# Kernel tuning notes

Measured on AMD Instinct MI355X. Metric: run time of the kernel, lower is better.

The kernel has to match this reference:

```python
import jax, jax.numpy as jnp
import numpy as np
from jax import lax

OUT = 7          # RoIAlign output size (7,7) per module
SR = 2           # sampling ratio (torchvision adaptive -1 made static for jit; see notes)
N_CLASSES = 21
N_ANCHORS = 2


def setup_inputs() -> dict:
    key = jax.random.key(0)
    ks = jax.random.split(key, 20)
    B, C, H, W = 2, 256, 100, 152
    K = 1024
    features = jax.random.normal(ks[0], (B, C, H, W), dtype=jnp.float32)
    # build valid ROIs [batch_idx, x1, y1, x2, y2] in feature-map coords (spatial_scale=1.0)
    bidx = jax.random.randint(ks[1], (K,), 0, B).astype(jnp.float32)
    cx = jax.random.uniform(ks[2], (K,)) * (W - 1)
    cy = jax.random.uniform(ks[3], (K,)) * (H - 1)
    bw = 4.0 + jax.random.uniform(ks[4], (K,)) * 60.0
    bh = 4.0 + jax.random.uniform(ks[5], (K,)) * 60.0
    x1 = jnp.clip(cx - bw / 2, 0.0, W - 1.0)
    x2 = jnp.clip(cx + bw / 2, 0.0, W - 1.0)
    y1 = jnp.clip(cy - bh / 2, 0.0, H - 1.0)
    y2 = jnp.clip(cy + bh / 2, 0.0, H - 1.0)
    rois = jnp.stack([bidx, x1, y1, x2, y2], axis=1)
    s = 0.05
    W1 = jax.random.normal(ks[6], (C, C, 3, 3), dtype=jnp.float32) * s
    b1 = jax.random.normal(ks[7], (C,), dtype=jnp.float32) * s
    W2 = jax.random.normal(ks[8], (C, C, 3, 3), dtype=jnp.float32) * s
    b2 = jax.random.normal(ks[9], (C,), dtype=jnp.float32) * s
    W3 = jax.random.normal(ks[10], (C, C, 3, 3), dtype=jnp.float32) * s
    b3 = jax.random.normal(ks[11], (C,), dtype=jnp.float32) * s
    W4 = jax.random.normal(ks[12], (C, C, 3, 3), dtype=jnp.float32) * s
    b4 = jax.random.normal(ks[13], (C,), dtype=jnp.float32) * s
    W5 = jax.random.normal(ks[14], (N_CLASSES * N_ANCHORS, C, 3, 3), dtype=jnp.float32) * s
    b5 = jax.random.normal(ks[15], (N_CLASSES * N_ANCHORS,), dtype=jnp.float32) * s
    return dict(features=features, rois=rois, W1=W1, b1=b1, W2=W2, b2=b2,
                W3=W3, b3=b3, W4=W4, b4=b4, W5=W5, b5=b5)


def roi_align(feat, rois):
    # feat [B,C,H,W], rois [K,5] -> [K,C,OUT,OUT]; bilinear, aligned=False semantics
    B, C, H, W = feat.shape
    b = rois[:, 0].astype(jnp.int32)                       # [K]
    x1, y1, x2, y2 = rois[:, 1], rois[:, 2], rois[:, 3], rois[:, 4]
    rw = jnp.maximum(x2 - x1, 1.0)
    rh = jnp.maximum(y2 - y1, 1.0)
    # sample point grid: OUT*SR samples per dim, centered in sub-bins
    offs = (jnp.arange(OUT * SR, dtype=feat.dtype) + 0.5) / SR  # in units of bins
    gy = y1[:, None] + offs[None, :] * (rh / OUT)[:, None]      # [K, S]
    gx = x1[:, None] + offs[None, :] * (rw / OUT)[:, None]      # [K, S]
    S = OUT * SR
    yy = jnp.broadcast_to(gy[:, :, None], (gy.shape[0], S, S)).reshape(-1, S * S)  # [K,P]
    xx = jnp.broadcast_to(gx[:, None, :], (gx.shape[0], S, S)).reshape(-1, S * S)
    valid = (yy > -1.0) & (yy < H) & (xx > -1.0) & (xx < W)
    yc = jnp.clip(yy, 0.0, H - 1.0)
    xc = jnp.clip(xx, 0.0, W - 1.0)
    y0 = jnp.clip(jnp.floor(yc), 0.0, H - 2.0)
    x0 = jnp.clip(jnp.floor(xc), 0.0, W - 2.0)
    wy = yc - y0
    wx = xc - x0
    y0i = y0.astype(jnp.int32); y1i = y0i + 1
    x0i = x0.astype(jnp.int32); x1i = x0i + 1
    bb = b[:, None]
    # irregular gathers: [K,P,C] each
    v00 = feat[bb, :, y0i, x0i]
    v01 = feat[bb, :, y0i, x1i]
    v10 = feat[bb, :, y1i, x0i]
    v11 = feat[bb, :, y1i, x1i]
    w00 = ((1 - wy) * (1 - wx))[..., None]
    w01 = ((1 - wy) * wx)[..., None]
    w10 = (wy * (1 - wx))[..., None]
    w11 = (wy * wx)[..., None]
    vals = v00 * w00 + v01 * w01 + v10 * w10 + v11 * w11   # [K,P,C]
    vals = jnp.where(valid[..., None], vals, 0.0)
    K = rois.shape[0]
    vals = vals.reshape(K, OUT, SR, OUT, SR, C).mean(axis=(2, 4))  # [K,OUT,OUT,C]
    return jnp.transpose(vals, (0, 3, 1, 2))               # [K,C,OUT,OUT]


def conv3x3(x, w, bias):
    y = lax.conv_general_dilated(x, w, (1, 1), ((1, 1), (1, 1)),
                                 dimension_numbers=('NCHW', 'OIHW', 'NCHW'))
    return y + bias[None, :, None, None]


def reference(features, rois, W1, b1, W2, b2, W3, b3, W4, b4, W5, b5):
    r = roi_align(features, rois)                # [K,256,7,7]
    h = jax.nn.relu(conv3x3(r, W1, b1))
    h = jax.nn.relu(conv3x3(h, W2, b2))
    h = jax.nn.relu(conv3x3(h, W3, b3))
    h = jax.nn.relu(conv3x3(h, W4, b4))
    out = conv3x3(h, W5, b5)                     # [K, n_classes*2, 7, 7]
    return out
```

## Files before the change

### kernel.cpp

```cpp
#include <hip/hip_runtime.h>
#include <hip/hip_bf16.h>

#define BB   2
#define CC   256
#define HH   100
#define WW   152
#define CO5  42

typedef short short8 __attribute__((ext_vector_type(8)));
typedef float f32x4 __attribute__((ext_vector_type(4)));

typedef unsigned int uint_t;
typedef unsigned short ushort_t;

__device__ __forceinline__ uint_t bf16_rne(float x) {
    uint_t u = __float_as_uint(x);
    return (u + 0x7fffu + ((u >> 16) & 1u)) >> 16;
}
__device__ __forceinline__ void split_bf16(float x, uint_t& h, uint_t& l) {
    h = bf16_rne(x);
    float hf = __uint_as_float(h << 16);
    l = bf16_rne(x - hf);
}

__global__ void ftrans_kernel(const float* __restrict__ f, float* __restrict__ ft) {
    __shared__ float tile[32][33];
    const int x0 = blockIdx.x * 32;
    const int c0 = blockIdx.y * 32;
    const int by = blockIdx.z;
    const int b = by / HH, y = by % HH;
    const int tx = threadIdx.x, ty = threadIdx.y;
    #pragma unroll
    for (int j = 0; j < 4; ++j) {
        int c = c0 + ty + j * 8;
        int x = x0 + tx;
        if (x < WW)
            tile[ty + j * 8][tx] = f[(((size_t)b * CC + c) * HH + y) * WW + x];
    }
    __syncthreads();
    #pragma unroll
    for (int j = 0; j < 4; ++j) {
        int x = x0 + ty + j * 8;
        int c = c0 + tx;
        if (x < WW)
            ft[(((size_t)b * HH + y) * WW + x) * CC + c] = tile[tx][ty + j * 8];
    }
}

__global__ void wprep_kernel(const float* __restrict__ W,
                             ushort_t* __restrict__ wh, ushort_t* __restrict__ wl) {
    int idx = blockIdx.x * 256 + threadIdx.x;
    int tap = idx >> 16;
    int rem = idx & 0xffff;
    int co = rem >> 8, ci = rem & 255;
    float v = W[(size_t)((co << 8) + ci) * 9 + tap];
    uint_t h, l; split_bf16(v, h, l);
    wh[idx] = (ushort_t)h;
    wl[idx] = (ushort_t)l;
}

__global__ void wprep5_kernel(const float* __restrict__ W,
                              ushort_t* __restrict__ wh, ushort_t* __restrict__ wl) {
    int idx = blockIdx.x * 256 + threadIdx.x;
    int tap = idx / 12288;
    int rem = idx % 12288;
    int co = rem >> 8, ci = rem & 255;
    float v = (co < CO5) ? W[(size_t)((co << 8) + ci) * 9 + tap] : 0.0f;
    uint_t h, l; split_bf16(v, h, l);
    wh[idx] = (ushort_t)h;
    wl[idx] = (ushort_t)l;
}

__global__ __launch_bounds__(256) void roialign_kernel(const float* __restrict__ ft,
                                                       const float* __restrict__ rois,
                                                       float* __restrict__ outb) {
    const int roi = blockIdx.x, t = threadIdx.x;
    const float bf = rois[roi * 5 + 0];
    const float x1 = rois[roi * 5 + 1];
    const float y1 = rois[roi * 5 + 2];
    const float x2 = rois[roi * 5 + 3];
    const float y2 = rois[roi * 5 + 4];
    const int b = (int)bf;
    const float rw = fmaxf(x2 - x1, 1.0f);
    const float rh = fmaxf(y2 - y1, 1.0f);
    const float stepy = rh / 7.0f;
    const float stepx = rw / 7.0f;
    const float* base = ft + (size_t)b * HH * WW * CC + t;

    for (int py = 0; py < 7; ++py) {
        for (int px = 0; px < 7; ++px) {
            float s = 0.0f;
            #pragma unroll
            for (int j = 0; j < 4; ++j) {
                const int syi = py * 2 + (j >> 1);
                const int sxi = px * 2 + (j & 1);
                float gy = y1 + ((float)syi + 0.5f) * 0.5f * stepy;
                float gx = x1 + ((float)sxi + 0.5f) * 0.5f * stepx;
                float yc = fminf(fmaxf(gy, 0.0f), (float)(HH - 1));
                float xc = fminf(fmaxf(gx, 0.0f), (float)(WW - 1));
                float y0f = fminf(floorf(yc), (float)(HH - 2));
                float x0f = fminf(floorf(xc), (float)(WW - 2));
                float wy = yc - y0f;
                float wx = xc - x0f;
                int y0 = (int)y0f, x0 = (int)x0f;
                const float* p = base + ((size_t)y0 * WW + x0) * CC;
                float v00 = p[0];
                float v01 = p[CC];
                float v10 = p[(size_t)WW * CC];
                float v11 = p[(size_t)WW * CC + CC];
                s += (1.0f - wy) * ((1.0f - wx) * v00 + wx * v01)
                   +          wy * ((1.0f - wx) * v10 + wx * v11);
            }
            outb[((size_t)roi * 49 + py * 7 + px) * CC + t] = 0.25f * s;
        }
    }
}

__device__ __forceinline__ void stage_roi(const float* __restrict__ src,
                                          ushort_t* Xh, ushort_t* Xl, int t) {
    const float2* s2 = (const float2*)src;
    const int half = t >> 7;
    const int cw = t & 127;
    #pragma unroll
    for (int i = 0; i < 25; ++i) {
        int row = i * 2 + half;
        if (row < 49) {
            float2 v = s2[row * 128 + cw];
            uint_t h0, l0, h1, l1;
            split_bf16(v.x, h0, l0);
            split_bf16(v.y, h1, l1);
            int addr = row * 512 + ((cw * 4) ^ ((row & 7) << 4));
            *(uint_t*)((char*)Xh + addr) = h0 | (h1 << 16);
            *(uint_t*)((char*)Xl + addr) = l0 | (l1 << 16);
        }
    }
    #pragma unroll
    for (int j = 0; j < 8; ++j) {
        int row = 49 + j * 2 + half;
        if (row < 64) {
            int addr = row * 512 + ((cw * 4) ^ ((row & 7) << 4));
            *(uint_t*)((char*)Xh + addr) = 0u;
            *(uint_t*)((char*)Xl + addr) = 0u;
        }
    }
}

__global__ __launch_bounds__(256, 2) void conv_mfma_kernel(
        const float* __restrict__ in, float* __restrict__ out,
        const ushort_t* __restrict__ wh, const ushort_t* __restrict__ wl,
        const float* __restrict__ bias, int relu) {
    __shared__ ushort_t X[2][64 * 256];
    const int roi = blockIdx.x, t = threadIdx.x;
    stage_roi(in + (size_t)roi * 49 * CC, X[0], X[1], t);
    __syncthreads();

    const int wv = t >> 6, l = t & 63;
    const int lr = l & 15;
    const int lk = l >> 4;
    const int n0 = wv * 64;

    f32x4 acc[4][4];
    #pragma unroll
    for (int a = 0; a < 4; ++a)
        #pragma unroll
        for (int b = 0; b < 4; ++b) acc[a][b] = {0.f, 0.f, 0.f, 0.f};

    const int bvoff = ((n0 + lr) * 256 + lk * 8) * 2;
    const char* Xhc = (const char*)X[0];
    const char* Xlc = (const char*)X[1];
    const int lk16 = lk * 16;

    for (int tap = 0; tap < 9; ++tap) {
        const int ky = tap / 3 - 1, kx = tap % 3 - 1;
        int arow[4], amask[4];
        #pragma unroll
        for (int mt = 0; mt < 4; ++mt) {
            int m = mt * 16 + lr;
            int py = m / 7, px = m - py * 7;
            int y = py + ky, x = px + kx;
            bool ok = (m < 49) && (y >= 0) && (y < 7) && (x >= 0) && (x < 7);
            int srow = ok ? (y * 7 + x) : 63;
            arow[mt]  = srow * 512;
            amask[mt] = (srow & 7) << 4;
        }
        const char* wht = (const char*)wh + tap * 131072;
        const char* wlt = (const char*)wl + tap * 131072;
        #pragma unroll
        for (int kc = 0; kc < 8; ++kc) {
            short8 ah[4], al[4];
            #pragma unroll
            for (int mt = 0; mt < 4; ++mt) {
                const int off = arow[mt] + ((lk16 + kc * 64) ^ amask[mt]);
                ah[mt] = *(const short8*)(Xhc + off);
                al[mt] = *(const short8*)(Xlc + off);
            }
            #pragma unroll
            for (int nt = 0; nt < 4; ++nt) {
                const int woff = bvoff + nt * 8192 + kc * 64;
                short8 bh = *(const short8*)(wht + woff);
                short8 bl = *(const short8*)(wlt + woff);
                #pragma unroll
                for (int mt = 0; mt < 4; ++mt)
                    acc[mt][nt] = __builtin_amdgcn_mfma_f32_16x16x32_bf16(ah[mt], bh, acc[mt][nt], 0, 0, 0);
                #pragma unroll
                for (int mt = 0; mt < 4; ++mt)
                    acc[mt][nt] = __builtin_amdgcn_mfma_f32_16x16x32_bf16(al[mt], bh, acc[mt][nt], 0, 0, 0);
                #pragma unroll
                for (int mt = 0; mt < 4; ++mt)
                    acc[mt][nt] = __builtin_amdgcn_mfma_f32_16x16x32_bf16(ah[mt], bl, acc[mt][nt], 0, 0, 0);
            }
        }
    }

    float* outp = out + (size_t)roi * 49 * CC;
    #pragma unroll
    for (int nt = 0; nt < 4; ++nt) {
        const int co = n0 + nt * 16 + lr;
        const float bv = bias[co];
        #pragma unroll
        for (int mt = 0; mt < 4; ++mt) {
            #pragma unroll
            for (int r = 0; r < 4; ++r) {
                int m = mt * 16 + lk * 4 + r;
                if (m < 49) {
                    float v = acc[mt][nt][r] + bv;
                    if (relu) v = fmaxf(v, 0.0f);
                    outp[m * 256 + co] = v;
                }
            }
        }
    }
}

__global__ __launch_bounds__(256, 2) void conv5_mfma_kernel(
        const float* __restrict__ in, float* __restrict__ out,
        const ushort_t* __restrict__ wh, const ushort_t* __restrict__ wl,
        const float* __restrict__ b5) {
    __shared__ ushort_t X[2][64 * 256];
    const int roi = blockIdx.x, t = threadIdx.x;
    stage_roi(in + (size_t)roi * 49 * CC, X[0], X[1], t);
    __syncthreads();

    const int wv = t >> 6, l = t & 63;
    const int lr = l & 15, lk = l >> 4;
    const int lk16 = lk * 16;

    f32x4 acc[4][3];
    #pragma unroll
    for (int a = 0; a < 4; ++a)
        #pragma unroll
        for (int b = 0; b < 3; ++b) acc[a][b] = {0.f, 0.f, 0.f, 0.f};

    const int bvoff = (lr * 256 + lk * 8) * 2;
    const char* Xhc = (const char*)X[0];
    const char* Xlc = (const char*)X[1];
    const int t0 = (wv == 0) ? 0 : (2 * wv + 1);
    const int t1 = 2 * wv + 3;

    for (int tap = t0; tap < t1; ++tap) {
        const int ky = tap / 3 - 1, kx = tap % 3 - 1;
        int arow[4], amask[4];
        #pragma unroll
        for (int mt = 0; mt < 4; ++mt) {
            int m = mt * 16 + lr;
            int py = m / 7, px = m - py * 7;
            int y = py + ky, x = px + kx;
            bool ok = (m < 49) && (y >= 0) && (y < 7) && (x >= 0) && (x < 7);
            int srow = ok ? (y * 7 + x) : 63;
            arow[mt]  = srow * 512;
            amask[mt] = (srow & 7) << 4;
        }
        const char* wht = (const char*)wh + tap * 24576;
        const char* wlt = (const char*)wl + tap * 24576;
        #pragma unroll
        for (int kc = 0; kc < 8; ++kc) {
            short8 ah[4], al[4];
            #pragma unroll
            for (int mt = 0; mt < 4; ++mt) {
                const int off = arow[mt] + ((lk16 + kc * 64) ^ amask[mt]);
                ah[mt] = *(const short8*)(Xhc + off);
                al[mt] = *(const short8*)(Xlc + off);
            }
            #pragma unroll
            for (int nt = 0; nt < 3; ++nt) {
                const int woff = bvoff + nt * 8192 + kc * 64;
                short8 bh = *(const short8*)(wht + woff);
                short8 bl = *(const short8*)(wlt + woff);
                #pragma unroll
                for (int mt = 0; mt < 4; ++mt)
                    acc[mt][nt] = __builtin_amdgcn_mfma_f32_16x16x32_bf16(ah[mt], bh, acc[mt][nt], 0, 0, 0);
                #pragma unroll
                for (int mt = 0; mt < 4; ++mt)
                    acc[mt][nt] = __builtin_amdgcn_mfma_f32_16x16x32_bf16(al[mt], bh, acc[mt][nt], 0, 0, 0);
                #pragma unroll
                for (int mt = 0; mt < 4; ++mt)
                    acc[mt][nt] = __builtin_amdgcn_mfma_f32_16x16x32_bf16(ah[mt], bl, acc[mt][nt], 0, 0, 0);
            }
        }
    }

    __syncthreads();
    float* P = (float*)X;
    #pragma unroll
    for (int nt = 0; nt < 3; ++nt)
        #pragma unroll
        for (int mt = 0; mt < 4; ++mt)
            #pragma unroll
            for (int r = 0; r < 4; ++r) {
                int m = mt * 16 + lk * 4 + r;
                P[wv * 3072 + m * 48 + nt * 16 + lr] = acc[mt][nt][r];
            }
    __syncthreads();

    for (int i = t; i < 49 * CO5; i += 256) {
        int n = i / 49, m = i % 49;
        float s = P[m * 48 + n] + P[3072 + m * 48 + n]
                + P[6144 + m * 48 + n] + P[9216 + m * 48 + n] + b5[n];
        out[(size_t)roi * (49 * CO5) + i] = s;
    }
}

extern "C" void kernel_launch(void* const* d_in, const int* in_sizes, int n_in,
                              void* d_out, int out_size, void* d_ws, size_t ws_size,
                              hipStream_t stream) {
    const float* features = (const float*)d_in[0];
    const float* rois     = (const float*)d_in[1];
    const float* W1 = (const float*)d_in[2];
    const float* b1 = (const float*)d_in[3];
    const float* W2 = (const float*)d_in[4];
    const float* b2 = (const float*)d_in[5];
    const float* W3 = (const float*)d_in[6];
    const float* b3 = (const float*)d_in[7];
    const float* W4 = (const float*)d_in[8];
    const float* b4 = (const float*)d_in[9];
    const float* W5 = (const float*)d_in[10];
    const float* b5 = (const float*)d_in[11];
    float* out = (float*)d_out;

    const int K = in_sizes[1] / 5;

    char* wsb = (char*)d_ws;
    float* ft   = (float*)wsb;
    float* buf0 = (float*)(wsb + 31129600);
    char* wb = wsb + 31129600 + 51380224;
    ushort_t* w1h = (ushort_t*)(wb + 0 * 1179648);
    ushort_t* w1l = (ushort_t*)(wb + 1 * 1179648);
    ushort_t* w2h = (ushort_t*)(wb + 2 * 1179648);
    ushort_t* w2l = (ushort_t*)(wb + 3 * 1179648);
    ushort_t* w3h = (ushort_t*)(wb + 4 * 1179648);
    ushort_t* w3l = (ushort_t*)(wb + 5 * 1179648);
    ushort_t* w4h = (ushort_t*)(wb + 6 * 1179648);
    ushort_t* w4l = (ushort_t*)(wb + 7 * 1179648);
    ushort_t* w5h = (ushort_t*)(wb + 8 * 1179648);
    ushort_t* w5l = (ushort_t*)(wb + 8 * 1179648 + 221184);

    {
        dim3 grid((WW + 31) / 32, CC / 32, BB * HH);
        dim3 block(32, 8);
        ftrans_kernel<<<grid, block, 0, stream>>>(features, ft);
    }
    wprep_kernel<<<2304, 256, 0, stream>>>(W1, w1h, w1l);
    wprep_kernel<<<2304, 256, 0, stream>>>(W2, w2h, w2l);
    wprep_kernel<<<2304, 256, 0, stream>>>(W3, w3h, w3l);
    wprep_kernel<<<2304, 256, 0, stream>>>(W4, w4h, w4l);
    wprep5_kernel<<<432, 256, 0, stream>>>(W5, w5h, w5l);
    roialign_kernel<<<K, 256, 0, stream>>>(ft, rois, buf0);
    conv_mfma_kernel<<<K, 256, 0, stream>>>(buf0, buf0, w1h, w1l, b1, 1);
    conv_mfma_kernel<<<K, 256, 0, stream>>>(buf0, buf0, w2h, w2l, b2, 1);
    conv_mfma_kernel<<<K, 256, 0, stream>>>(buf0, buf0, w3h, w3l, b3, 1);
    conv_mfma_kernel<<<K, 256, 0, stream>>>(buf0, buf0, w4h, w4l, b4, 1);
    conv5_mfma_kernel<<<K, 256, 0, stream>>>(buf0, out, w5h, w5l, b5);
}
```

Measured before the change: 1.349 ms.

## Fuse RoIAlign into first conv and shrink LDS tile for higher occupancy

RoIAlign sampling now runs directly inside the first conv kernel, writing bf16 hi/lo splits straight into shared memory, so the standalone roialign kernel and its global write/read round trip go away. The shared tile shrinks from 64 to 50 rows, with a single zero row used for padding taps. Launch bounds rise from 2 to 3 blocks per CU so more blocks can be resident. RoIAlign now loads two channels per thread as float2. Risks: register pressure under the tighter launch bounds, and the fused kernel's gather latency now sits in front of its MFMA work.

```diff
diff --git a/kernel.cpp b/kernel.cpp
--- a/kernel.cpp
+++ b/kernel.cpp
@@ -6,6 +6,9 @@
 #define HH   100
 #define WW   152
 #define CO5  42
+
+#define XROWS 50
+#define ZROW  49
 
 typedef short short8 __attribute__((ext_vector_type(8)));
 typedef float f32x4 __attribute__((ext_vector_type(4)));
@@ -71,10 +74,33 @@
     wl[idx] = (ushort_t)l;
 }
 
-__global__ __launch_bounds__(256) void roialign_kernel(const float* __restrict__ ft,
-                                                       const float* __restrict__ rois,
-                                                       float* __restrict__ outb) {
-    const int roi = blockIdx.x, t = threadIdx.x;
+__device__ __forceinline__ void stage_roi(const float* __restrict__ src,
+                                          ushort_t* Xh, ushort_t* Xl, int t) {
+    const float2* s2 = (const float2*)src;
+    const int half = t >> 7;
+    const int cw = t & 127;
+    #pragma unroll
+    for (int i = 0; i < 25; ++i) {
+        int row = i * 2 + half;
+        int addr = row * 512 + ((cw * 4) ^ ((row & 7) << 4));
+        uint_t ph = 0u, pl = 0u;
+        if (row < 49) {
+            float2 v = s2[row * 128 + cw];
+            uint_t h0, l0, h1, l1;
+            split_bf16(v.x, h0, l0);
+            split_bf16(v.y, h1, l1);
+            ph = h0 | (h1 << 16);
+            pl = l0 | (l1 << 16);
+        }
+        *(uint_t*)((char*)Xh + addr) = ph;
+        *(uint_t*)((char*)Xl + addr) = pl;
+    }
+}
+
+__device__ __forceinline__ void stage_roi_align(const float* __restrict__ ft,
+                                                const float* __restrict__ rois,
+                                                ushort_t* Xh, ushort_t* Xl,
+                                                int roi, int t) {
     const float bf = rois[roi * 5 + 0];
     const float x1 = rois[roi * 5 + 1];
     const float y1 = rois[roi * 5 + 2];
@@ -85,11 +111,19 @@
     const float rh = fmaxf(y2 - y1, 1.0f);
     const float stepy = rh / 7.0f;
     const float stepx = rw / 7.0f;
-    const float* base = ft + (size_t)b * HH * WW * CC + t;
-
-    for (int py = 0; py < 7; ++py) {
-        for (int px = 0; px < 7; ++px) {
-            float s = 0.0f;
+
+    const int half = t >> 7;
+    const int cw = t & 127;
+    const float* base = ft + (size_t)b * HH * WW * CC + cw * 2;
+
+    #pragma unroll
+    for (int i = 0; i < 25; ++i) {
+        int row = i * 2 + half;
+        int addr = row * 512 + ((cw * 4) ^ ((row & 7) << 4));
+        uint_t ph = 0u, pl = 0u;
+        if (row < 49) {
+            int py = row / 7, px = row - (row / 7) * 7;
+            float sx = 0.0f, sy_ = 0.0f;
             #pragma unroll
             for (int j = 0; j < 4; ++j) {
                 const int syi = py * 2 + (j >> 1);
@@ -104,60 +138,38 @@
                 float wx = xc - x0f;
                 int y0 = (int)y0f, x0 = (int)x0f;
                 const float* p = base + ((size_t)y0 * WW + x0) * CC;
-                float v00 = p[0];
-                float v01 = p[CC];
-                float v10 = p[(size_t)WW * CC];
-                float v11 = p[(size_t)WW * CC + CC];
-                s += (1.0f - wy) * ((1.0f - wx) * v00 + wx * v01)
-                   +          wy * ((1.0f - wx) * v10 + wx * v11);
-            }
-            outb[((size_t)roi * 49 + py * 7 + px) * CC + t] = 0.25f * s;
-        }
-    }
-}
-
-__device__ __forceinline__ void stage_roi(const float* __restrict__ src,
-                                          ushort_t* Xh, ushort_t* Xl, int t) {
-    const float2* s2 = (const float2*)src;
-    const int half = t >> 7;
-    const int cw = t & 127;
-    #pragma unroll
-    for (int i = 0; i < 25; ++i) {
-        int row = i * 2 + half;
-        if (row < 49) {
-            float2 v = s2[row * 128 + cw];
+                float2 v00 = *(const float2*)(p);
+                float2 v01 = *(const float2*)(p + CC);
+                float2 v10 = *(const float2*)(p + (size_t)WW * CC);
+                float2 v11 = *(const float2*)(p + (size_t)WW * CC + CC);
+                float w00 = (1.0f - wy) * (1.0f - wx);
+                float w01 = (1.0f - wy) * wx;
+                float w10 = wy * (1.0f - wx);
+                float w11 = wy * wx;
+                sx  += w00 * v00.x + w01 * v01.x + w10 * v10.x + w11 * v11.x;
+                sy_ += w00 * v00.y + w01 * v01.y + w10 * v10.y + w11 * v11.y;
+            }
             uint_t h0, l0, h1, l1;
-            split_bf16(v.x, h0, l0);
-            split_bf16(v.y, h1, l1);
-            int addr = row * 512 + ((cw * 4) ^ ((row & 7) << 4));
-            *(uint_t*)((char*)Xh + addr) = h0 | (h1 << 16);
-            *(uint_t*)((char*)Xl + addr) = l0 | (l1 << 16);
-        }
-    }
-    #pragma unroll
-    for (int j = 0; j < 8; ++j) {
-        int row = 49 + j * 2 + half;
-        if (row < 64) {
-            int addr = row * 512 + ((cw * 4) ^ ((row & 7) << 4));
-            *(uint_t*)((char*)Xh + addr) = 0u;
-            *(uint_t*)((char*)Xl + addr) = 0u;
-        }
-    }
-}
-
-__global__ __launch_bounds__(256, 2) void conv_mfma_kernel(
-        const float* __restrict__ in, float* __restrict__ out,
+            split_bf16(0.25f * sx, h0, l0);
+            split_bf16(0.25f * sy_, h1, l1);
+            ph = h0 | (h1 << 16);
+            pl = l0 | (l1 << 16);
+        }
+        *(uint_t*)((char*)Xh + addr) = ph;
+        *(uint_t*)((char*)Xl + addr) = pl;
+    }
+}
+
+__device__ __forceinline__ void conv_core_256(
+        const char* Xhc, const char* Xlc,
         const ushort_t* __restrict__ wh, const ushort_t* __restrict__ wl,
-        const float* __restrict__ bias, int relu) {
-    __shared__ ushort_t X[2][64 * 256];
-    const int roi = blockIdx.x, t = threadIdx.x;
-    stage_roi(in + (size_t)roi * 49 * CC, X[0], X[1], t);
-    __syncthreads();
-
+        const float* __restrict__ bias, float* __restrict__ outp,
+        int relu, int t) {
     const int wv = t >> 6, l = t & 63;
     const int lr = l & 15;
     const int lk = l >> 4;
     const int n0 = wv * 64;
+    const int lk16 = lk * 16;
 
     f32x4 acc[4][4];
     #pragma unroll
@@ -166,9 +178,6 @@
         for (int b = 0; b < 4; ++b) acc[a][b] = {0.f, 0.f, 0.f, 0.f};
 
     const int bvoff = ((n0 + lr) * 256 + lk * 8) * 2;
-    const char* Xhc = (const char*)X[0];
-    const char* Xlc = (const char*)X[1];
-    const int lk16 = lk * 16;
 
     for (int tap = 0; tap < 9; ++tap) {
         const int ky = tap / 3 - 1, kx = tap % 3 - 1;
@@ -176,10 +185,10 @@
         #pragma unroll
         for (int mt = 0; mt < 4; ++mt) {
             int m = mt * 16 + lr;
-            int py = m / 7, px = m - py * 7;
+            int py = m / 7, px = m - (m / 7) * 7;
             int y = py + ky, x = px + kx;
             bool ok = (m < 49) && (y >= 0) && (y < 7) && (x >= 0) && (x < 7);
-            int srow = ok ? (y * 7 + x) : 63;
+            int srow = ok ? (y * 7 + x) : ZROW;
             arow[mt]  = srow * 512;
             amask[mt] = (srow & 7) << 4;
         }
@@ -212,7 +221,6 @@
         }
     }
 
-    float* outp = out + (size_t)roi * 49 * CC;
     #pragma unroll
     for (int nt = 0; nt < 4; ++nt) {
         const int co = n0 + nt * 16 + lr;
@@ -232,11 +240,36 @@
     }
 }
 
-__global__ __launch_bounds__(256, 2) void conv5_mfma_kernel(
+__global__ __launch_bounds__(256, 3) void conv1_fused_kernel(
+        const float* __restrict__ ft, const float* __restrict__ rois,
+        float* __restrict__ out,
+        const ushort_t* __restrict__ wh, const ushort_t* __restrict__ wl,
+        const float* __restrict__ bias) {
+    __shared__ ushort_t X[2][XROWS * 256];
+    const int roi = blockIdx.x, t = threadIdx.x;
+    stage_roi_align(ft, rois, X[0], X[1], roi, t);
+    __syncthreads();
+    conv_core_256((const char*)X[0], (const char*)X[1], wh, wl, bias,
+                  out + (size_t)roi * 49 * CC, 1, t);
+}
+
+__global__ __launch_bounds__(256, 3) void conv_mfma_kernel(
+        const float* __restrict__ in, float* __restrict__ out,
+        const ushort_t* __restrict__ wh, const ushort_t* __restrict__ wl,
+        const float* __restrict__ bias) {
+    __shared__ ushort_t X[2][XROWS * 256];
+    const int roi = blockIdx.x, t = threadIdx.x;
+    stage_roi(in + (size_t)roi * 49 * CC, X[0], X[1], t);
+    __syncthreads();
+    conv_core_256((const char*)X[0], (const char*)X[1], wh, wl, bias,
+                  out + (size_t)roi * 49 * CC, 1, t);
+}
+
+__global__ __launch_bounds__(256, 3) void conv5_mfma_kernel(
         const float* __restrict__ in, float* __restrict__ out,
         const ushort_t* __restrict__ wh, const ushort_t* __restrict__ wl,
         const float* __restrict__ b5) {
-    __shared__ ushort_t X[2][64 * 256];
+    __shared__ ushort_t X[2][XROWS * 256];
     const int roi = blockIdx.x, t = threadIdx.x;
     stage_roi(in + (size_t)roi * 49 * CC, X[0], X[1], t);
     __syncthreads();
@@ -263,10 +296,10 @@
         #pragma unroll
         for (int mt = 0; mt < 4; ++mt) {
             int m = mt * 16 + lr;
-            int py = m / 7, px = m - py * 7;
+            int py = m / 7, px = m - (m / 7) * 7;
             int y = py + ky, x = px + kx;
             bool ok = (m < 49) && (y >= 0) && (y < 7) && (x >= 0) && (x < 7);
-            int srow = ok ? (y * 7 + x) : 63;
+            int srow = ok ? (y * 7 + x) : ZROW;
             arow[mt]  = srow * 512;
             amask[mt] = (srow & 7) << 4;
         }
@@ -364,10 +397,9 @@
     wprep_kernel<<<2304, 256, 0, stream>>>(W3, w3h, w3l);
     wprep_kernel<<<2304, 256, 0, stream>>>(W4, w4h, w4l);
     wprep5_kernel<<<432, 256, 0, stream>>>(W5, w5h, w5l);
-    roialign_kernel<<<K, 256, 0, stream>>>(ft, rois, buf0);
-    conv_mfma_kernel<<<K, 256, 0, stream>>>(buf0, buf0, w1h, w1l, b1, 1);
-    conv_mfma_kernel<<<K, 256, 0, stream>>>(buf0, buf0, w2h, w2l, b2, 1);
-    conv_mfma_kernel<<<K, 256, 0, stream>>>(buf0, buf0, w3h, w3l, b3, 1);
-    conv_mfma_kernel<<<K, 256, 0, stream>>>(buf0, buf0, w4h, w4l, b4, 1);
+    conv1_fused_kernel<<<K, 256, 0, stream>>>(ft, rois, buf0, w1h, w1l, b1);
+    conv_mfma_kernel<<<K, 256, 0, stream>>>(buf0, buf0, w2h, w2l, b2);
+    conv_mfma_kernel<<<K, 256, 0, stream>>>(buf0, buf0, w3h, w3l, b3);
+    conv_mfma_kernel<<<K, 256, 0, stream>>>(buf0, buf0, w4h, w4l, b4);
     conv5_mfma_kernel<<<K, 256, 0, stream>>>(buf0, out, w5h, w5l, b5);
 }
```

Result: slower. 2.181 ms (+61.7%).
